# Optimization experiments

Measured on AMD Instinct MI355X. Metric: run time of the kernel, lower is better.

## Reference

```python
import jax, jax.numpy as jnp
import numpy as np

B, N, S, T, D, H, DH, FF = 16, 300, 300, 77, 512, 8, 64, 2048
L = T + S + N
XPOS_SCALE_BASE = 512.0


def _ln(v):
    m = v.mean(-1, keepdims=True)
    var = v.var(-1, keepdims=True)
    return (v - m) * jax.lax.rsqrt(var + 1e-6)


def _rms(v, g):
    return v * jax.lax.rsqrt(jnp.mean(v * v, axis=-1, keepdims=True) + 1e-6) * g


def _rotate_half(v):
    half = v.shape[-1] // 2
    v2 = v.reshape(v.shape[:-1] + (half, 2))
    return jnp.stack([-v2[..., 1], v2[..., 0]], axis=-1).reshape(v.shape)


def _rope_xpos(q, k):
    # lucidrains RotaryEmbedding(dim=64, use_xpos=True).rotate_queries_and_keys
    Dh = q.shape[-1]
    Lq = q.shape[-2]
    inv = 1.0 / (10000.0 ** (jnp.arange(0, Dh, 2, dtype=jnp.float32) / Dh))
    t = jnp.arange(Lq, dtype=jnp.float32)
    ang = jnp.repeat(t[:, None] * inv[None, :], 2, axis=-1)  # [L, Dh]
    base = (jnp.arange(0, Dh, 2, dtype=jnp.float32) + 0.4 * Dh) / (1.4 * Dh)
    power = (t - Lq // 2) / XPOS_SCALE_BASE
    scale = jnp.repeat(base[None, :] ** power[:, None], 2, axis=-1)  # [L, Dh]
    cos, sin = jnp.cos(ang), jnp.sin(ang)
    qo = q * (cos * scale) + _rotate_half(q) * (sin * scale)
    ko = k * (cos / scale) + _rotate_half(k) * (sin / scale)
    return qo, ko


def _fwd(x, src, txt, temb, Wqkv, bqkv, Wo, bo, gqk, Wada, bada, Wff1, bff1, Wff2, bff2, pos_q, pos_k, valid):
    Bb = x.shape[0]
    # AdaLayerNormZero modulation per stream (0=hidden, 1=source, 2=text)
    ada = jnp.einsum('bd,sde->sbe', jax.nn.silu(temb), Wada) + bada[:, None, :]  # [3,B,6D]
    sh_a, sc_a, g_a, sh_m, sc_m, g_m = jnp.split(ada, 6, axis=-1)  # each [3,B,D]

    streams = [x, src, txt]
    qs, ks_, vs = [], [], []
    for i, s_ in enumerate(streams):
        n = _ln(s_) * (1.0 + sc_a[i][:, None, :]) + sh_a[i][:, None, :]
        q = (n @ Wqkv[i, 0] + bqkv[i, 0]).reshape(Bb, -1, H, DH).transpose(0, 2, 1, 3)
        k = (n @ Wqkv[i, 1] + bqkv[i, 1]).reshape(Bb, -1, H, DH).transpose(0, 2, 1, 3)
        v = (n @ Wqkv[i, 2] + bqkv[i, 2]).reshape(Bb, -1, H, DH).transpose(0, 2, 1, 3)
        q = _rms(q, gqk[i, 0])
        k = _rms(k, gqk[i, 1])
        qs.append(q); ks_.append(k); vs.append(v)

    # rotary (xpos) on motion streams, learned pos-embed on text stream
    q0, k0 = _rope_xpos(qs[0], ks_[0])
    q1, k1 = _rope_xpos(qs[1], ks_[1])
    q2 = qs[2] + pos_q[None, None, :, :]
    k2 = ks_[2] + pos_k[None, None, :, :]

    # concat order: [text, source, hidden]
    q = jnp.concatenate([q2, q1, q0], axis=2)
    k = jnp.concatenate([k2, k1, k0], axis=2)
    v = jnp.concatenate([vs[2], vs[1], vs[0]], axis=2)

    Lt = q.shape[2]
    vm = valid.astype(jnp.float32)
    mask = (vm[:, :, None] * vm[:, None, :]) > 0
    mask = mask | jnp.eye(Lt, dtype=bool)[None]  # compute_boolean_matrix
    bias = jnp.where(mask, 0.0, -jnp.inf)[:, None, :, :]

    scores = jnp.einsum('bhld,bhmd->bhlm', q, k) / jnp.sqrt(jnp.float32(DH)) + bias
    att = jax.nn.softmax(scores, axis=-1)
    o = jnp.einsum('bhlm,bhmd->bhld', att, v).transpose(0, 2, 1, 3).reshape(Bb, Lt, H * DH)

    Tl, Sl = txt.shape[1], src.shape[1]
    attouts = [o[:, Tl + Sl:], o[:, Tl:Tl + Sl], o[:, :Tl]]  # hidden, source, text
    outs = []
    for i, (s_, ao) in enumerate(zip(streams, attouts)):
        a = ao @ Wo[i] + bo[i]
        h = s_ + g_a[i][:, None, :] * a
        n2 = _ln(h) * (1.0 + sc_m[i][:, None, :]) + sh_m[i][:, None, :]
        u = n2 @ Wff1[i] + bff1[i]
        lin, gate = jnp.split(u, 2, axis=-1)
        ff = (lin * jax.nn.gelu(gate, approximate=False)) @ Wff2[i] + bff2[i]
        outs.append(h + g_m[i][:, None, :] * ff)
    # return concat [text, source, hidden]
    return jnp.concatenate([outs[2], outs[1], outs[0]], axis=1)


def setup_inputs() -> dict:
    key = jax.random.key(0)
    ks = jax.random.split(key, 20)
    p = lambda k, shp: jax.random.normal(k, shp, jnp.float32) * 0.02
    return {
        'x': jax.random.normal(ks[0], (B, N, D), jnp.float32),
        'src': jax.random.normal(ks[1], (B, S, D), jnp.float32),
        'txt': jax.random.normal(ks[2], (B, T, D), jnp.float32),
        'temb': jax.random.normal(ks[3], (B, D), jnp.float32),
        'Wqkv': p(ks[4], (3, 3, D, D)),
        'bqkv': p(ks[5], (3, 3, D)),
        'Wo': p(ks[6], (3, D, D)),
        'bo': p(ks[7], (3, D)),
        'gqk': jnp.ones((3, 2, DH), jnp.float32),
        'Wada': p(ks[8], (3, D, 6 * D)),
        'bada': p(ks[9], (3, 6 * D)),
        'Wff1': p(ks[10], (3, D, 2 * FF)),
        'bff1': p(ks[11], (3, 2 * FF)),
        'Wff2': p(ks[12], (3, FF, D)),
        'bff2': p(ks[13], (3, D)),
        'pos_q': p(ks[14], (T, DH)),
        'pos_k': p(ks[15], (T, DH)),
        'valid': jax.random.randint(ks[16], (B, L), 0, 2, dtype=jnp.int32),
    }


def reference(x, src, txt, temb, Wqkv, bqkv, Wo, bo, gqk, Wada, bada, Wff1, bff1, Wff2, bff2, pos_q, pos_k, valid):
    return _fwd(x, src, txt, temb, Wqkv, bqkv, Wo, bo, gqk, Wada, bada, Wff1, bff1, Wff2, bff2, pos_q, pos_k, valid)
```

## Files before the change

### kernel.cpp

```cpp
#include <hip/hip_runtime.h>
#include <math.h>

#define DEV __device__ __forceinline__

typedef short bf8 __attribute__((ext_vector_type(8)));
typedef float f32x4 __attribute__((ext_vector_type(4)));

#define TOK 10832

DEV unsigned short f2bf(float f) {
  union { float f; unsigned u; } x; x.f = f;
  unsigned r = x.u + 0x7fffu + ((x.u >> 16) & 1u);
  return (unsigned short)(r >> 16);
}
DEV float bf2f(unsigned short h) {
  union { unsigned u; float f; } x; x.u = ((unsigned)h) << 16; return x.f;
}
DEV unsigned cvtpk(float lo, float hi) {
  unsigned r;
  asm("v_cvt_pk_bf16_f32 %0, %1, %2" : "=v"(r) : "v"(lo), "v"(hi));
  return r;
}
DEV void decode_row(int row, int& s, int& b, int& p) {
  if (row < 4800)      { s = 0; b = row / 300; p = row - b * 300; }
  else if (row < 9600) { s = 1; int r = row - 4800; b = r / 300; p = r - b * 300; }
  else                 { s = 2; int r = row - 9600; b = r / 77;  p = r - b * 77; }
}
DEV f32x4 MFMA(bf8 a, bf8 b, f32x4 c) {
  return __builtin_amdgcn_mfma_f32_16x16x32_bf16(a, b, c, 0, 0, 0);
}
DEV void gld16(const unsigned short* g, unsigned short* l) {
  __builtin_amdgcn_global_load_lds((const __attribute__((address_space(1))) unsigned int*)g,
                                   (__attribute__((address_space(3))) unsigned int*)l,
                                   16, 0, 0);
}
DEV void vmdrain() { asm volatile("s_waitcnt vmcnt(0)" ::: "memory"); }

__global__ __launch_bounds__(256) void k_transpose(const float* __restrict__ src,
                                                   unsigned short* __restrict__ dst,
                                                   int R, int C, long sstride, long dstride) {
  __shared__ float t[32][33];
  const float* s = src + (long)blockIdx.z * sstride;
  unsigned short* d = dst + (long)blockIdx.z * dstride;
  int c0 = blockIdx.x * 32, r0 = blockIdx.y * 32;
  int tx = threadIdx.x, ty = threadIdx.y;
  #pragma unroll
  for (int i = ty; i < 32; i += 8) t[i][tx] = s[(long)(r0 + i) * C + c0 + tx];
  __syncthreads();
  #pragma unroll
  for (int i = ty; i < 32; i += 8) d[(long)(c0 + i) * R + r0 + tx] = f2bf(t[tx][i]);
}

__global__ __launch_bounds__(256) void k_ada1(const float* __restrict__ temb,
    const float* __restrict__ Wada, float* __restrict__ part) {
  __shared__ float st[16][64];
  int s = blockIdx.y, kc = blockIdx.z;
  int e = blockIdx.x * 256 + threadIdx.x;
  int d0 = kc * 64;
  for (int i = threadIdx.x; i < 16 * 64; i += 256) {
    int b = i >> 6, d = i & 63;
    float v = temb[b * 512 + d0 + d];
    st[b][d] = v / (1.f + __expf(-v));
  }
  __syncthreads();
  float acc[16];
  #pragma unroll
  for (int b = 0; b < 16; b++) acc[b] = 0.f;
  const float* wp = Wada + (long)s * 512 * 3072 + (long)d0 * 3072 + e;
  for (int d = 0; d < 64; d++) {
    float wv = wp[(long)d * 3072];
    #pragma unroll
    for (int b = 0; b < 16; b++) acc[b] += st[b][d] * wv;
  }
  float* pp = part + (((long)kc * 3 + s) * 16) * 3072 + e;
  #pragma unroll
  for (int b = 0; b < 16; b++) pp[(long)b * 3072] = acc[b];
}

__global__ __launch_bounds__(256) void k_ada2(const float* __restrict__ part,
    const float* __restrict__ bada, float* __restrict__ ada) {
  int idx = blockIdx.x * 256 + threadIdx.x;
  int e = idx % 3072, sb = idx / 3072, s = sb >> 4;
  float a = bada[s * 3072 + e];
  #pragma unroll
  for (int kc = 0; kc < 8; kc++) a += part[((long)kc * 48 + sb) * 3072 + e];
  ada[idx] = a;
}

__global__ __launch_bounds__(256) void k_rope_tab(float* __restrict__ rc,
    float* __restrict__ rs, float* __restrict__ rsc) {
  int i = blockIdx.x * 256 + threadIdx.x;
  if (i >= 300 * 32) return;
  int p = i >> 5, f = i & 31;
  float inv = powf(10000.f, -(2.f * f) / 64.f);
  float ang = (float)p * inv;
  float base = (2.f * f + 25.6f) / 89.6f;
  float pw = (float)(p - 150) * (1.f / 512.f);
  rc[i] = cosf(ang);
  rs[i] = sinf(ang);
  rsc[i] = powf(base, pw);
}

__global__ __launch_bounds__(256) void k_padzero(unsigned short* __restrict__ qb,
    unsigned short* __restrict__ kb, unsigned short* __restrict__ vtb) {
  int bh = blockIdx.x, t = threadIdx.x;
  for (int i = t; i < 27 * 64; i += 256) {
    int r = 677 + (i >> 6), c = i & 63;
    long idx = ((long)bh * 704 + r) * 64 + c;
    qb[idx] = 0; kb[idx] = 0;
  }
  for (int i = t; i < 64 * 27; i += 256) {
    int r = i / 27, c = 677 + (i - r * 27);
    vtb[((long)bh * 64 + r) * 704 + c] = 0;
  }
}

__global__ __launch_bounds__(256) void k_lnmod(const float* __restrict__ xp,
    const float* __restrict__ sp, const float* __restrict__ tp,
    const float* __restrict__ hbuf, const float* __restrict__ ada,
    unsigned short* __restrict__ outp, int chunk) {
  int row = blockIdx.x;
  int s, b, p; decode_row(row, s, b, p);
  const float* in;
  if (hbuf) in = hbuf + (long)row * 512;
  else {
    const float* basep = (s == 0) ? xp : (s == 1) ? sp : tp;
    int len = (s == 2) ? 77 : 300;
    in = basep + ((long)b * len + p) * 512;
  }
  int t = threadIdx.x;
  float v0 = in[t], v1 = in[t + 256];
  float s1 = v0 + v1, s2 = v0 * v0 + v1 * v1;
  #pragma unroll
  for (int d = 32; d; d >>= 1) { s1 += __shfl_xor(s1, d); s2 += __shfl_xor(s2, d); }
  __shared__ float r1[4], r2[4];
  int wid = t >> 6, lane = t & 63;
  if (lane == 0) { r1[wid] = s1; r2[wid] = s2; }
  __syncthreads();
  float S = r1[0] + r1[1] + r1[2] + r1[3];
  float Q = r2[0] + r2[1] + r2[2] + r2[3];
  float mean = S * (1.f / 512.f);
  float var = Q * (1.f / 512.f) - mean * mean;
  float rstd = rsqrtf(var + 1e-6f);
  const float* ap = ada + ((long)s * 16 + b) * 3072 + chunk * 512;
  float sh0 = ap[t], sh1 = ap[t + 256];
  float sc0 = ap[512 + t], sc1 = ap[512 + t + 256];
  long ob = (long)row * 512;
  outp[ob + t]       = f2bf((v0 - mean) * rstd * (1.f + sc0) + sh0);
  outp[ob + t + 256] = f2bf((v1 - mean) * rstd * (1.f + sc1) + sh1);
}

template <int EPI>
__global__ __launch_bounds__(256) void k_gemm128(const unsigned short* __restrict__ A,
    const unsigned short* __restrict__ Wt, const float* __restrict__ bias,
    float* __restrict__ outF, unsigned short* __restrict__ outB,
    const float* __restrict__ hread, const float* __restrict__ ada,
    const float* __restrict__ xp, const float* __restrict__ sp, const float* __restrict__ tp,
    int K, int N) {
  int s = blockIdx.z;
  int mt = blockIdx.y;
  int Mtiles = (s == 2) ? 10 : 38;
  if (mt >= Mtiles) return;
  int Ms = (s == 2) ? 1232 : 4800;
  int rowbase = s * 4800;
  int m0 = mt * 128, n0 = blockIdx.x * 128;
  __shared__ unsigned short As[2][4096];
  __shared__ unsigned short Bs[2][4096];
  int tid = threadIdx.x;
  int w = tid >> 6, lane = tid & 63;
  int wr = w >> 1, wc = w & 1;
  int l16 = lane & 15, lg = lane >> 4;
  const unsigned short* Ag = A + (long)rowbase * K;
  const unsigned short* Bg = Wt + (long)s * N * K;
  int lrow = lane >> 2, lcol = (lane & 3) * 8;
  int ar[2], br[2];
  #pragma unroll
  for (int rnd = 0; rnd < 2; rnd++) {
    int rr = (w * 2 + rnd) * 16 + lrow;
    int a_ = m0 + rr; if (a_ >= Ms) a_ = Ms - 1;
    ar[rnd] = a_;
    br[rnd] = n0 + rr;
  }
  f32x4 acc[4][4];
  #pragma unroll
  for (int i = 0; i < 4; i++)
    #pragma unroll
    for (int j = 0; j < 4; j++) acc[i][j] = (f32x4){0.f, 0.f, 0.f, 0.f};
  #pragma unroll
  for (int rnd = 0; rnd < 2; rnd++) {
    gld16(Ag + (long)ar[rnd] * K + lcol, &As[0][(w * 2 + rnd) * 512]);
    gld16(Bg + (long)br[rnd] * K + lcol, &Bs[0][(w * 2 + rnd) * 512]);
  }
  vmdrain();
  __syncthreads();
  int buf = 0;
  for (int k0 = 0; k0 < K; k0 += 32) {
    int nx = k0 + 32;
    if (nx < K) {
      #pragma unroll
      for (int rnd = 0; rnd < 2; rnd++) {
        gld16(Ag + (long)ar[rnd] * K + nx + lcol, &As[buf ^ 1][(w * 2 + rnd) * 512]);
        gld16(Bg + (long)br[rnd] * K + nx + lcol, &Bs[buf ^ 1][(w * 2 + rnd) * 512]);
      }
    }
    bf8 af[4], bv[4];
    #pragma unroll
    for (int i = 0; i < 4; i++) {
      af[i] = *(const bf8*)&As[buf][(wr * 64 + i * 16 + l16) * 32 + lg * 8];
      bv[i] = *(const bf8*)&Bs[buf][(wc * 64 + i * 16 + l16) * 32 + lg * 8];
    }
    #pragma unroll
    for (int i = 0; i < 4; i++)
      #pragma unroll
      for (int j = 0; j < 4; j++)
        acc[i][j] = MFMA(af[i], bv[j], acc[i][j]);
    vmdrain();
    __syncthreads();
    buf ^= 1;
  }
  #pragma unroll
  for (int i = 0; i < 4; i++) {
    #pragma unroll
    for (int r = 0; r < 4; r++) {
      int rloc = m0 + wr * 64 + i * 16 + lg * 4 + r;
      if (rloc >= Ms) continue;
      int grow = rowbase + rloc;
      int b, p;
      if (s == 2) { b = rloc / 77;  p = rloc - b * 77; }
      else        { b = rloc / 300; p = rloc - b * 300; }
      #pragma unroll
      for (int j = 0; j < 4; j++) {
        int col = n0 + wc * 64 + j * 16 + l16;
        float v = acc[i][j][r] + bias[s * N + col];
        if constexpr (EPI == 0) {
          outB[(long)grow * 1536 + col] = f2bf(v);
        } else if constexpr (EPI == 1) {
          const float* basep = (s == 0) ? xp : (s == 1) ? sp : tp;
          int len = (s == 2) ? 77 : 300;
          float iv = basep[((long)b * len + p) * 512 + col];
          float ga = ada[((long)s * 16 + b) * 3072 + 1024 + col];
          outF[(long)grow * 512 + col] = iv + ga * v;
        } else {
          float hv = hread[(long)grow * 512 + col];
          float gm = ada[((long)s * 16 + b) * 3072 + 2560 + col];
          int l = ((s == 0) ? 377 : (s == 1) ? 77 : 0) + p;
          outF[((long)b * 677 + l) * 512 + col] = hv + gm * v;
        }
      }
    }
  }
}

__global__ __launch_bounds__(256) void k_geglu128(const unsigned short* __restrict__ A,
    const unsigned short* __restrict__ Wt, const float* __restrict__ bias,
    unsigned short* __restrict__ gout) {
  int s = blockIdx.z;
  int mt = blockIdx.y;
  int Mtiles = (s == 2) ? 10 : 38;
  if (mt >= Mtiles) return;
  int Ms = (s == 2) ? 1232 : 4800;
  int rowbase = s * 4800;
  int m0 = mt * 128, n0 = blockIdx.x * 64;
  __shared__ unsigned short As[2][4096];
  __shared__ unsigned short Bl[2][2048];
  __shared__ unsigned short Bg[2][2048];
  int tid = threadIdx.x;
  int w = tid >> 6, lane = tid & 63;
  int l16 = lane & 15, lg = lane >> 4;
  const unsigned short* Ag = A + (long)rowbase * 512;
  const unsigned short* Ws = Wt + (long)s * 4096 * 512;
  int lrow = lane >> 2, lcol = (lane & 3) * 8;
  int ar[2];
  #pragma unroll
  for (int rnd = 0; rnd < 2; rnd++) {
    int a_ = m0 + (w * 2 + rnd) * 16 + lrow; if (a_ >= Ms) a_ = Ms - 1;
    ar[rnd] = a_;
  }
  int blr = n0 + w * 16 + lrow;
  int bgr = 2048 + n0 + w * 16 + lrow;
  f32x4 accl[2][4], accg[2][4];
  #pragma unroll
  for (int i = 0; i < 2; i++)
    #pragma unroll
    for (int j = 0; j < 4; j++) {
      accl[i][j] = (f32x4){0.f, 0.f, 0.f, 0.f};
      accg[i][j] = (f32x4){0.f, 0.f, 0.f, 0.f};
    }
  #pragma unroll
  for (int rnd = 0; rnd < 2; rnd++)
    gld16(Ag + (long)ar[rnd] * 512 + lcol, &As[0][(w * 2 + rnd) * 512]);
  gld16(Ws + (long)blr * 512 + lcol, &Bl[0][w * 512]);
  gld16(Ws + (long)bgr * 512 + lcol, &Bg[0][w * 512]);
  vmdrain();
  __syncthreads();
  int buf = 0;
  for (int k0 = 0; k0 < 512; k0 += 32) {
    int nx = k0 + 32;
    if (nx < 512) {
      #pragma unroll
      for (int rnd = 0; rnd < 2; rnd++)
        gld16(Ag + (long)ar[rnd] * 512 + nx + lcol, &As[buf ^ 1][(w * 2 + rnd) * 512]);
      gld16(Ws + (long)blr * 512 + nx + lcol, &Bl[buf ^ 1][w * 512]);
      gld16(Ws + (long)bgr * 512 + nx + lcol, &Bg[buf ^ 1][w * 512]);
    }
    bf8 af[2], bl[4], bg[4];
    #pragma unroll
    for (int i = 0; i < 2; i++)
      af[i] = *(const bf8*)&As[buf][(w * 32 + i * 16 + l16) * 32 + lg * 8];
    #pragma unroll
    for (int j = 0; j < 4; j++) {
      bl[j] = *(const bf8*)&Bl[buf][(j * 16 + l16) * 32 + lg * 8];
      bg[j] = *(const bf8*)&Bg[buf][(j * 16 + l16) * 32 + lg * 8];
    }
    #pragma unroll
    for (int i = 0; i < 2; i++)
      #pragma unroll
      for (int j = 0; j < 4; j++) {
        accl[i][j] = MFMA(af[i], bl[j], accl[i][j]);
        accg[i][j] = MFMA(af[i], bg[j], accg[i][j]);
      }
    vmdrain();
    __syncthreads();
    buf ^= 1;
  }
  #pragma unroll
  for (int i = 0; i < 2; i++) {
    #pragma unroll
    for (int r = 0; r < 4; r++) {
      int rloc = m0 + w * 32 + i * 16 + lg * 4 + r;
      if (rloc >= Ms) continue;
      int grow = rowbase + rloc;
      #pragma unroll
      for (int j = 0; j < 4; j++) {
        int col = n0 + j * 16 + l16;
        float lv = accl[i][j][r] + bias[s * 4096 + col];
        float gv = accg[i][j][r] + bias[s * 4096 + 2048 + col];
        float g  = lv * 0.5f * gv * (1.f + erff(gv * 0.70710678118654752f));
        gout[(long)grow * 2048 + col] = f2bf(g);
      }
    }
  }
}

__global__ __launch_bounds__(256) void k_rmsrope(const unsigned short* __restrict__ qkv,
    const float* __restrict__ gqk, const float* __restrict__ posq, const float* __restrict__ posk,
    const float* __restrict__ rcos, const float* __restrict__ rsin, const float* __restrict__ rscl,
    unsigned short* __restrict__ qb, unsigned short* __restrict__ kb,
    unsigned short* __restrict__ vtb) {
  int gw = (blockIdx.x * 256 + threadIdx.x) >> 6;
  int lane = threadIdx.x & 63;
  int token = gw >> 3, h = gw & 7;
  if (token >= TOK) return;
  int s, b, p; decode_row(token, s, b, p);
  long base = (long)token * 1536 + h * 64 + lane;
  float q = bf2f(qkv[base]);
  float k = bf2f(qkv[base + 512]);
  float v = bf2f(qkv[base + 1024]);
  float sq = q * q, sk = k * k;
  #pragma unroll
  for (int d = 32; d; d >>= 1) { sq += __shfl_xor(sq, d); sk += __shfl_xor(sk, d); }
  q *= rsqrtf(sq * (1.f / 64.f) + 1e-6f) * gqk[s * 128 + lane];
  k *= rsqrtf(sk * (1.f / 64.f) + 1e-6f) * gqk[s * 128 + 64 + lane];
  int l;
  if (s == 2) {
    l = p;
    q += posq[p * 64 + lane];
    k += posk[p * 64 + lane];
  } else {
    l = (s == 1 ? 77 : 377) + p;
    int pr = lane >> 1;
    float c = rcos[p * 32 + pr], sn = rsin[p * 32 + pr], sc = rscl[p * 32 + pr];
    float qo = __shfl_xor(q, 1), ko = __shfl_xor(k, 1);
    float sgn = (lane & 1) ? 1.f : -1.f;
    q = (q * c + sgn * qo * sn) * sc;
    k = (k * c + sgn * ko * sn) / sc;
  }
  long bh = (long)(b * 8 + h);
  long qi = (bh * 704 + l) * 64 + lane;
  qb[qi] = f2bf(q);
  kb[qi] = f2bf(k);
  vtb[(bh * 64 + lane) * 704 + l] = f2bf(v);
}

__global__ __launch_bounds__(512, 8) void k_attn(const unsigned short* __restrict__ qb,
    const unsigned short* __restrict__ kb, const unsigned short* __restrict__ vtb,
    const int* __restrict__ valid, unsigned short* __restrict__ ob) {
  __shared__ unsigned short Kb[2][4096];
  __shared__ unsigned short Vb[2][4096];
  __shared__ unsigned char maskv[704];
  int f0 = blockIdx.x;
  int fp = (f0 & 7) * 96 + (f0 >> 3);
  int bh = fp / 6, qtile = fp - bh * 6;
  int b = bh >> 3, h = bh & 7;
  int tid = threadIdx.x;
  for (int i = tid; i < 704; i += 512)
    maskv[i] = (i < 677) ? (unsigned char)(valid[b * 677 + i] != 0) : (unsigned char)0;
  int w = tid >> 6, lane = tid & 63;
  int l16 = lane & 15, lg = lane >> 4;
  int qt = qtile * 128 + w * 16;
  int qrow = qt + l16;
  int qrc = qrow > 703 ? 703 : qrow;
  const unsigned short* qbase = qb + (long)bh * 704 * 64;
  const unsigned short* kbase = kb + (long)bh * 704 * 64;
  const unsigned short* vbase = vtb + (long)bh * 64 * 704;
  bf8 qf0 = *(const bf8*)(qbase + qrc * 64 + lg * 8);
  bf8 qf1 = *(const bf8*)(qbase + qrc * 64 + 32 + lg * 8);
  int scol = (((lane & 7) << 4) ^ ((lane >> 3) << 4)) >> 1;
  int srow = w * 8 + (lane >> 3);
  const unsigned short* ksrc = kbase + srow * 64 + scol;
  const unsigned short* vsrc = vbase + srow * 704 + scol;
  unsigned short* kd0 = &Kb[0][w * 512];
  unsigned short* kd1 = &Kb[1][w * 512];
  unsigned short* vd0 = &Vb[0][w * 512];
  unsigned short* vd1 = &Vb[1][w * 512];
  gld16(ksrc, kd0);
  gld16(vsrc, vd0);
  vmdrain();
  __syncthreads();
  int mq = maskv[qrc];
  int sw = (l16 & 7) << 4;
  float lsum = 0.f;
  f32x4 Oc[4];
  #pragma unroll
  for (int df = 0; df < 4; df++) Oc[df] = (f32x4){0.f, 0.f, 0.f, 0.f};
  union U { bf8 v; unsigned u[4]; uint2 d[2]; };
  int buf = 0;
  for (int t = 0; t < 11; t++) {
    if (t < 10) {
      int ktn = (t + 1) * 64;
      gld16(ksrc + ktn * 64, buf ? kd0 : kd1);
      gld16(vsrc + ktn, buf ? vd0 : vd1);
    }
    int kt = t * 64;
    const unsigned short* Kc = Kb[buf];
    const unsigned short* Vc = Vb[buf];
    float psum = 0.f;
    unsigned pk[4][2];
    #pragma unroll
    for (int f = 0; f < 4; f++) {
      int row = f * 16 + l16;
      f32x4 sa = (f32x4){0.f, 0.f, 0.f, 0.f};
      sa = MFMA(*(const bf8*)&Kc[(row * 128 + ((lg * 16) ^ sw)) >> 1], qf0, sa);
      sa = MFMA(*(const bf8*)&Kc[(row * 128 + ((lg * 16 + 64) ^ sw)) >> 1], qf1, sa);
      unsigned mw = *(const unsigned*)&maskv[kt + f * 16 + lg * 4];
      float pr[4];
      #pragma unroll
      for (int r = 0; r < 4; r++) {
        int key = kt + f * 16 + lg * 4 + r;
        bool ok = ((mq & (mw >> (8 * r))) & 1) || (key == qrow);
        float sv = ok ? fmaf(sa[r], 0.125f, -20.f) : -1e30f;
        float pv = __expf(sv);
        pr[r] = pv;
        psum += pv;
      }
      pk[f][0] = cvtpk(pr[0], pr[1]);
      pk[f][1] = cvtpk(pr[2], pr[3]);
    }
    psum += __shfl_xor(psum, 16);
    psum += __shfl_xor(psum, 32);
    lsum += psum;
    #pragma unroll
    for (int c = 0; c < 2; c++) {
      U pu;
      pu.u[0] = pk[2 * c][0]; pu.u[1] = pk[2 * c][1];
      pu.u[2] = pk[2 * c + 1][0]; pu.u[3] = pk[2 * c + 1][1];
      #pragma unroll
      for (int df = 0; df < 4; df++) {
        int row = df * 16 + l16;
        U vu;
        vu.d[0] = *(const uint2*)&Vc[(row * 128 + ((c * 64 + lg * 8) ^ sw)) >> 1];
        vu.d[1] = *(const uint2*)&Vc[(row * 128 + ((c * 64 + lg * 8 + 32) ^ sw)) >> 1];
        Oc[df] = MFMA(vu.v, pu.v, Oc[df]);
      }
    }
    vmdrain();
    __syncthreads();
    buf ^= 1;
  }
  if (qrow < 677) {
    float inv = 1.f / fmaxf(lsum, 1e-30f);
    int l = qrow;
    int orow = (l < 77) ? 9600 + b * 77 + l
             : (l < 377) ? 4800 + b * 300 + (l - 77)
                         : b * 300 + (l - 377);
    unsigned short* op = ob + (long)orow * 512 + h * 64;
    #pragma unroll
    for (int df = 0; df < 4; df++) {
      uint2 st;
      st.x = cvtpk(Oc[df][0] * inv, Oc[df][1] * inv);
      st.y = cvtpk(Oc[df][2] * inv, Oc[df][3] * inv);
      *(uint2*)(op + df * 16 + lg * 4) = st;
    }
  }
}

extern "C" void kernel_launch(void* const* d_in, const int* in_sizes, int n_in,
                              void* d_out, int out_size, void* d_ws, size_t ws_size,
                              hipStream_t stream) {
  const float* xp   = (const float*)d_in[0];
  const float* sp   = (const float*)d_in[1];
  const float* tp   = (const float*)d_in[2];
  const float* temb = (const float*)d_in[3];
  const float* Wqkv = (const float*)d_in[4];
  const float* bqkv = (const float*)d_in[5];
  const float* Wo   = (const float*)d_in[6];
  const float* bo   = (const float*)d_in[7];
  const float* gqk  = (const float*)d_in[8];
  const float* Wada = (const float*)d_in[9];
  const float* bada = (const float*)d_in[10];
  const float* Wff1 = (const float*)d_in[11];
  const float* bff1 = (const float*)d_in[12];
  const float* Wff2 = (const float*)d_in[13];
  const float* bff2 = (const float*)d_in[14];
  const float* posq = (const float*)d_in[15];
  const float* posk = (const float*)d_in[16];
  const int*   valid= (const int*)d_in[17];
  float* out = (float*)d_out;

  char* w = (char*)d_ws;
  size_t off = 0;
  auto take = [&](size_t bytes) -> char* {
    char* p = w + off;
    off = (off + bytes + 255) & ~(size_t)255;
    return p;
  };
  unsigned short* wqkvT = (unsigned short*)take(3UL * 1536 * 512 * 2);
  unsigned short* woT   = (unsigned short*)take(3UL * 512 * 512 * 2);
  unsigned short* wff1T = (unsigned short*)take(3UL * 4096 * 512 * 2);
  unsigned short* wff2T = (unsigned short*)take(3UL * 512 * 2048 * 2);
  float*          adab  = (float*)take(3UL * 16 * 3072 * 4);
  float*          adap  = (float*)take(8UL * 3 * 16 * 3072 * 4);
  float*          rcosb = (float*)take(300UL * 32 * 4);
  float*          rsinb = (float*)take(300UL * 32 * 4);
  float*          rsclb = (float*)take(300UL * 32 * 4);
  unsigned short* nbuf  = (unsigned short*)take((size_t)TOK * 512 * 2);
  unsigned short* qkvb  = (unsigned short*)take((size_t)TOK * 1536 * 2);
  unsigned short* qbf   = (unsigned short*)take(16UL * 8 * 704 * 64 * 2);
  unsigned short* kbf   = (unsigned short*)take(16UL * 8 * 704 * 64 * 2);
  unsigned short* vtb   = (unsigned short*)take(16UL * 8 * 64 * 704 * 2);
  unsigned short* obuf  = (unsigned short*)take((size_t)TOK * 512 * 2);
  float*          hb    = (float*)take((size_t)TOK * 512 * 4);
  unsigned short* n2b   = (unsigned short*)take((size_t)TOK * 512 * 2);
  unsigned short* gbuf  = (unsigned short*)take((size_t)TOK * 2048 * 2);
  (void)ws_size; (void)in_sizes; (void)n_in; (void)out_size;

  k_transpose<<<dim3(16, 16, 9), dim3(32, 8), 0, stream>>>(Wqkv, wqkvT, 512, 512, 262144L, 262144L);
  k_transpose<<<dim3(16, 16, 3), dim3(32, 8), 0, stream>>>(Wo, woT, 512, 512, 262144L, 262144L);
  k_transpose<<<dim3(128, 16, 3), dim3(32, 8), 0, stream>>>(Wff1, wff1T, 512, 4096, 2097152L, 2097152L);
  k_transpose<<<dim3(16, 64, 3), dim3(32, 8), 0, stream>>>(Wff2, wff2T, 2048, 512, 1048576L, 1048576L);
  k_ada1<<<dim3(12, 3, 8), 256, 0, stream>>>(temb, Wada, adap);
  k_ada2<<<576, 256, 0, stream>>>(adap, bada, adab);
  k_rope_tab<<<38, 256, 0, stream>>>(rcosb, rsinb, rsclb);
  k_padzero<<<128, 256, 0, stream>>>(qbf, kbf, vtb);
  k_lnmod<<<TOK, 256, 0, stream>>>(xp, sp, tp, nullptr, adab, nbuf, 0);
  k_gemm128<0><<<dim3(12, 38, 3), 256, 0, stream>>>(nbuf, wqkvT, bqkv, nullptr, qkvb, nullptr,
                                                    adab, xp, sp, tp, 512, 1536);
  k_rmsrope<<<21664, 256, 0, stream>>>(qkvb, gqk, posq, posk, rcosb, rsinb, rsclb, qbf, kbf, vtb);
  k_attn<<<768, 512, 0, stream>>>(qbf, kbf, vtb, valid, obuf);
  k_gemm128<1><<<dim3(4, 38, 3), 256, 0, stream>>>(obuf, woT, bo, hb, nullptr, nullptr,
                                                   adab, xp, sp, tp, 512, 512);
  k_lnmod<<<TOK, 256, 0, stream>>>(xp, sp, tp, hb, adab, n2b, 3);
  k_geglu128<<<dim3(32, 38, 3), 256, 0, stream>>>(n2b, wff1T, bff1, gbuf);
  k_gemm128<2><<<dim3(4, 38, 3), 256, 0, stream>>>(gbuf, wff2T, bff2, out, nullptr, hb,
                                                   adab, xp, sp, tp, 2048, 512);
}
```

Baseline: 470.8 us.

## Merge prep kernels into one launch and triple-buffer GEMM LDS pipelines

```diff
diff --git a/kernel.cpp b/kernel.cpp
--- a/kernel.cpp
+++ b/kernel.cpp
@@ -35,46 +35,99 @@
                                    16, 0, 0);
 }
 DEV void vmdrain() { asm volatile("s_waitcnt vmcnt(0)" ::: "memory"); }
-
-__global__ __launch_bounds__(256) void k_transpose(const float* __restrict__ src,
-                                                   unsigned short* __restrict__ dst,
-                                                   int R, int C, long sstride, long dstride) {
-  __shared__ float t[32][33];
-  const float* s = src + (long)blockIdx.z * sstride;
-  unsigned short* d = dst + (long)blockIdx.z * dstride;
-  int c0 = blockIdx.x * 32, r0 = blockIdx.y * 32;
-  int tx = threadIdx.x, ty = threadIdx.y;
-  #pragma unroll
-  for (int i = ty; i < 32; i += 8) t[i][tx] = s[(long)(r0 + i) * C + c0 + tx];
+DEV void pipe_bar4() {
+  asm volatile("s_waitcnt vmcnt(4) lgkmcnt(0)" ::: "memory");
+  __builtin_amdgcn_s_barrier();
+  __builtin_amdgcn_sched_barrier(0);
+}
+DEV void pipe_bar0() {
+  asm volatile("s_waitcnt vmcnt(0) lgkmcnt(0)" ::: "memory");
+  __builtin_amdgcn_s_barrier();
+  __builtin_amdgcn_sched_barrier(0);
+}
+
+DEV void tr32(const float* __restrict__ src, unsigned short* __restrict__ dst,
+              int R, int C, int cx, int cy, int tid, float* sh) {
+  int tx = tid & 31, ty = tid >> 5;
+  int c0 = cx * 32, r0 = cy * 32;
+  #pragma unroll
+  for (int i = ty; i < 32; i += 8) sh[i * 33 + tx] = src[(long)(r0 + i) * C + c0 + tx];
   __syncthreads();
   #pragma unroll
-  for (int i = ty; i < 32; i += 8) d[(long)(c0 + i) * R + r0 + tx] = f2bf(t[tx][i]);
-}
-
-__global__ __launch_bounds__(256) void k_ada1(const float* __restrict__ temb,
-    const float* __restrict__ Wada, float* __restrict__ part) {
-  __shared__ float st[16][64];
-  int s = blockIdx.y, kc = blockIdx.z;
-  int e = blockIdx.x * 256 + threadIdx.x;
-  int d0 = kc * 64;
-  for (int i = threadIdx.x; i < 16 * 64; i += 256) {
-    int b = i >> 6, d = i & 63;
-    float v = temb[b * 512 + d0 + d];
-    st[b][d] = v / (1.f + __expf(-v));
-  }
-  __syncthreads();
-  float acc[16];
-  #pragma unroll
-  for (int b = 0; b < 16; b++) acc[b] = 0.f;
-  const float* wp = Wada + (long)s * 512 * 3072 + (long)d0 * 3072 + e;
-  for (int d = 0; d < 64; d++) {
-    float wv = wp[(long)d * 3072];
-    #pragma unroll
-    for (int b = 0; b < 16; b++) acc[b] += st[b][d] * wv;
-  }
-  float* pp = part + (((long)kc * 3 + s) * 16) * 3072 + e;
-  #pragma unroll
-  for (int b = 0; b < 16; b++) pp[(long)b * 3072] = acc[b];
+  for (int i = ty; i < 32; i += 8) dst[(long)(c0 + i) * R + r0 + tx] = f2bf(sh[tx * 33 + i]);
+}
+
+__global__ __launch_bounds__(256) void k_prep(
+    const float* __restrict__ Wqkv, const float* __restrict__ Wo,
+    const float* __restrict__ Wff1, const float* __restrict__ Wff2,
+    unsigned short* __restrict__ wqkvT, unsigned short* __restrict__ woT,
+    unsigned short* __restrict__ wff1T, unsigned short* __restrict__ wff2T,
+    unsigned short* __restrict__ qb, unsigned short* __restrict__ kb,
+    unsigned short* __restrict__ vtb,
+    float* __restrict__ rc, float* __restrict__ rs, float* __restrict__ rsc,
+    const float* __restrict__ temb, const float* __restrict__ Wada,
+    float* __restrict__ part) {
+  __shared__ float sh[32 * 33];
+  int i = blockIdx.x, tid = threadIdx.x;
+  if (i < 2304) {
+    int z = i >> 8, r = i & 255;
+    tr32(Wqkv + (long)z * 262144, wqkvT + (long)z * 262144, 512, 512, r & 15, r >> 4, tid, sh);
+  } else if (i < 3072) {
+    int j = i - 2304; int z = j >> 8, r = j & 255;
+    tr32(Wo + (long)z * 262144, woT + (long)z * 262144, 512, 512, r & 15, r >> 4, tid, sh);
+  } else if (i < 9216) {
+    int j = i - 3072; int z = j >> 11, r = j & 2047;
+    tr32(Wff1 + (long)z * 2097152, wff1T + (long)z * 2097152, 512, 4096, r & 127, r >> 7, tid, sh);
+  } else if (i < 12288) {
+    int j = i - 9216; int z = j >> 10, r = j & 1023;
+    tr32(Wff2 + (long)z * 1048576, wff2T + (long)z * 1048576, 2048, 512, r & 15, r >> 4, tid, sh);
+  } else if (i < 12416) {
+    int bh = i - 12288;
+    for (int q = tid; q < 27 * 64; q += 256) {
+      int r = 677 + (q >> 6), c = q & 63;
+      long idx = ((long)bh * 704 + r) * 64 + c;
+      qb[idx] = 0; kb[idx] = 0;
+    }
+    for (int q = tid; q < 64 * 27; q += 256) {
+      int r = q / 27, c = 677 + (q - r * 27);
+      vtb[((long)bh * 64 + r) * 704 + c] = 0;
+    }
+  } else if (i < 12454) {
+    int q = (i - 12416) * 256 + tid;
+    if (q < 300 * 32) {
+      int p = q >> 5, f = q & 31;
+      float inv = powf(10000.f, -(2.f * f) / 64.f);
+      float ang = (float)p * inv;
+      float base = (2.f * f + 25.6f) / 89.6f;
+      float pw = (float)(p - 150) * (1.f / 512.f);
+      rc[q] = cosf(ang);
+      rs[q] = sinf(ang);
+      rsc[q] = powf(base, pw);
+    }
+  } else {
+    int j = i - 12454;
+    int ex = j % 12, rest = j / 12, s = rest % 3, kc = rest / 3;
+    int d0 = kc * 64;
+    for (int q = tid; q < 16 * 64; q += 256) {
+      int b = q >> 6, d = q & 63;
+      float v = temb[b * 512 + d0 + d];
+      sh[(b << 6) + d] = v / (1.f + __expf(-v));
+    }
+    __syncthreads();
+    int e = ex * 256 + tid;
+    float acc[16];
+    #pragma unroll
+    for (int b = 0; b < 16; b++) acc[b] = 0.f;
+    const float* wp = Wada + (long)s * 512 * 3072 + (long)d0 * 3072 + e;
+    for (int d = 0; d < 64; d++) {
+      float wv = wp[(long)d * 3072];
+      #pragma unroll
+      for (int b = 0; b < 16; b++) acc[b] += sh[(b << 6) + d] * wv;
+    }
+    float* pp = part + (((long)kc * 3 + s) * 16) * 3072 + e;
+    #pragma unroll
+    for (int b = 0; b < 16; b++) pp[(long)b * 3072] = acc[b];
+  }
 }
 
 __global__ __launch_bounds__(256) void k_ada2(const float* __restrict__ part,
@@ -85,34 +138,6 @@
   #pragma unroll
   for (int kc = 0; kc < 8; kc++) a += part[((long)kc * 48 + sb) * 3072 + e];
   ada[idx] = a;
-}
-
-__global__ __launch_bounds__(256) void k_rope_tab(float* __restrict__ rc,
-    float* __restrict__ rs, float* __restrict__ rsc) {
-  int i = blockIdx.x * 256 + threadIdx.x;
-  if (i >= 300 * 32) return;
-  int p = i >> 5, f = i & 31;
-  float inv = powf(10000.f, -(2.f * f) / 64.f);
-  float ang = (float)p * inv;
-  float base = (2.f * f + 25.6f) / 89.6f;
-  float pw = (float)(p - 150) * (1.f / 512.f);
-  rc[i] = cosf(ang);
-  rs[i] = sinf(ang);
-  rsc[i] = powf(base, pw);
-}
-
-__global__ __launch_bounds__(256) void k_padzero(unsigned short* __restrict__ qb,
-    unsigned short* __restrict__ kb, unsigned short* __restrict__ vtb) {
-  int bh = blockIdx.x, t = threadIdx.x;
-  for (int i = t; i < 27 * 64; i += 256) {
-    int r = 677 + (i >> 6), c = i & 63;
-    long idx = ((long)bh * 704 + r) * 64 + c;
-    qb[idx] = 0; kb[idx] = 0;
-  }
-  for (int i = t; i < 64 * 27; i += 256) {
-    int r = i / 27, c = 677 + (i - r * 27);
-    vtb[((long)bh * 64 + r) * 704 + c] = 0;
-  }
 }
 
 __global__ __launch_bounds__(256) void k_lnmod(const float* __restrict__ xp,
@@ -164,8 +189,8 @@
   int Ms = (s == 2) ? 1232 : 4800;
   int rowbase = s * 4800;
   int m0 = mt * 128, n0 = blockIdx.x * 128;
-  __shared__ unsigned short As[2][4096];
-  __shared__ unsigned short Bs[2][4096];
+  __shared__ unsigned short As[3][4096];
+  __shared__ unsigned short Bs[3][4096];
   int tid = threadIdx.x;
   int w = tid >> 6, lane = tid & 63;
   int wr = w >> 1, wc = w & 1;
@@ -181,42 +206,40 @@
     ar[rnd] = a_;
     br[rnd] = n0 + rr;
   }
+  auto stage = [&](int kt, int bufi) {
+    #pragma unroll
+    for (int rnd = 0; rnd < 2; rnd++) {
+      gld16(Ag + (long)ar[rnd] * K + kt + lcol, &As[bufi][(w * 2 + rnd) * 512]);
+      gld16(Bg + (long)br[rnd] * K + kt + lcol, &Bs[bufi][(w * 2 + rnd) * 512]);
+    }
+  };
   f32x4 acc[4][4];
   #pragma unroll
   for (int i = 0; i < 4; i++)
     #pragma unroll
     for (int j = 0; j < 4; j++) acc[i][j] = (f32x4){0.f, 0.f, 0.f, 0.f};
-  #pragma unroll
-  for (int rnd = 0; rnd < 2; rnd++) {
-    gld16(Ag + (long)ar[rnd] * K + lcol, &As[0][(w * 2 + rnd) * 512]);
-    gld16(Bg + (long)br[rnd] * K + lcol, &Bs[0][(w * 2 + rnd) * 512]);
-  }
-  vmdrain();
-  __syncthreads();
-  int buf = 0;
-  for (int k0 = 0; k0 < K; k0 += 32) {
-    int nx = k0 + 32;
-    if (nx < K) {
-      #pragma unroll
-      for (int rnd = 0; rnd < 2; rnd++) {
-        gld16(Ag + (long)ar[rnd] * K + nx + lcol, &As[buf ^ 1][(w * 2 + rnd) * 512]);
-        gld16(Bg + (long)br[rnd] * K + nx + lcol, &Bs[buf ^ 1][(w * 2 + rnd) * 512]);
-      }
+  int nt = K >> 5;
+  stage(0, 0);
+  stage(32, 1);
+  int bi = 0;
+  for (int t = 0; t < nt; ++t) {
+    if (t == nt - 1) pipe_bar0(); else pipe_bar4();
+    if (t + 2 < nt) {
+      int b2 = bi + 2; if (b2 >= 3) b2 -= 3;
+      stage((t + 2) << 5, b2);
     }
     bf8 af[4], bv[4];
     #pragma unroll
     for (int i = 0; i < 4; i++) {
-      af[i] = *(const bf8*)&As[buf][(wr * 64 + i * 16 + l16) * 32 + lg * 8];
-      bv[i] = *(const bf8*)&Bs[buf][(wc * 64 + i * 16 + l16) * 32 + lg * 8];
+      af[i] = *(const bf8*)&As[bi][(wr * 64 + i * 16 + l16) * 32 + lg * 8];
+      bv[i] = *(const bf8*)&Bs[bi][(wc * 64 + i * 16 + l16) * 32 + lg * 8];
     }
     #pragma unroll
     for (int i = 0; i < 4; i++)
       #pragma unroll
       for (int j = 0; j < 4; j++)
         acc[i][j] = MFMA(af[i], bv[j], acc[i][j]);
-    vmdrain();
-    __syncthreads();
-    buf ^= 1;
+    bi = (bi + 1 == 3) ? 0 : bi + 1;
   }
   #pragma unroll
   for (int i = 0; i < 4; i++) {
@@ -261,9 +284,9 @@
   int Ms = (s == 2) ? 1232 : 4800;
   int rowbase = s * 4800;
   int m0 = mt * 128, n0 = blockIdx.x * 64;
-  __shared__ unsigned short As[2][4096];
-  __shared__ unsigned short Bl[2][2048];
-  __shared__ unsigned short Bg[2][2048];
+  __shared__ unsigned short As[3][4096];
+  __shared__ unsigned short Bl[3][2048];
+  __shared__ unsigned short Bg[3][2048];
   int tid = threadIdx.x;
   int w = tid >> 6, lane = tid & 63;
   int l16 = lane & 15, lg = lane >> 4;
@@ -278,6 +301,13 @@
   }
   int blr = n0 + w * 16 + lrow;
   int bgr = 2048 + n0 + w * 16 + lrow;
+  auto stage = [&](int kt, int bufi) {
+    #pragma unroll
+    for (int rnd = 0; rnd < 2; rnd++)
+      gld16(Ag + (long)ar[rnd] * 512 + kt + lcol, &As[bufi][(w * 2 + rnd) * 512]);
+    gld16(Ws + (long)blr * 512 + kt + lcol, &Bl[bufi][w * 512]);
+    gld16(Ws + (long)bgr * 512 + kt + lcol, &Bg[bufi][w * 512]);
+  };
   f32x4 accl[2][4], accg[2][4];
   #pragma unroll
   for (int i = 0; i < 2; i++)
@@ -286,31 +316,23 @@
       accl[i][j] = (f32x4){0.f, 0.f, 0.f, 0.f};
       accg[i][j] = (f32x4){0.f, 0.f, 0.f, 0.f};
     }
-  #pragma unroll
-  for (int rnd = 0; rnd < 2; rnd++)
-    gld16(Ag + (long)ar[rnd] * 512 + lcol, &As[0][(w * 2 + rnd) * 512]);
-  gld16(Ws + (long)blr * 512 + lcol, &Bl[0][w * 512]);
-  gld16(Ws + (long)bgr * 512 + lcol, &Bg[0][w * 512]);
-  vmdrain();
-  __syncthreads();
-  int buf = 0;
-  for (int k0 = 0; k0 < 512; k0 += 32) {
-    int nx = k0 + 32;
-    if (nx < 512) {
-      #pragma unroll
-      for (int rnd = 0; rnd < 2; rnd++)
-        gld16(Ag + (long)ar[rnd] * 512 + nx + lcol, &As[buf ^ 1][(w * 2 + rnd) * 512]);
-      gld16(Ws + (long)blr * 512 + nx + lcol, &Bl[buf ^ 1][w * 512]);
-      gld16(Ws + (long)bgr * 512 + nx + lcol, &Bg[buf ^ 1][w * 512]);
+  stage(0, 0);
+  stage(32, 1);
+  int bi = 0;
+  for (int t = 0; t < 16; ++t) {
+    if (t == 15) pipe_bar0(); else pipe_bar4();
+    if (t + 2 < 16) {
+      int b2 = bi + 2; if (b2 >= 3) b2 -= 3;
+      stage((t + 2) << 5, b2);
     }
     bf8 af[2], bl[4], bg[4];
     #pragma unroll
     for (int i = 0; i < 2; i++)
-      af[i] = *(const bf8*)&As[buf][(w * 32 + i * 16 + l16) * 32 + lg * 8];
+      af[i] = *(const bf8*)&As[bi][(w * 32 + i * 16 + l16) * 32 + lg * 8];
     #pragma unroll
     for (int j = 0; j < 4; j++) {
-      bl[j] = *(const bf8*)&Bl[buf][(j * 16 + l16) * 32 + lg * 8];
-      bg[j] = *(const bf8*)&Bg[buf][(j * 16 + l16) * 32 + lg * 8];
+      bl[j] = *(const bf8*)&Bl[bi][(j * 16 + l16) * 32 + lg * 8];
+      bg[j] = *(const bf8*)&Bg[bi][(j * 16 + l16) * 32 + lg * 8];
     }
     #pragma unroll
     for (int i = 0; i < 2; i++)
@@ -319,9 +341,7 @@
         accl[i][j] = MFMA(af[i], bl[j], accl[i][j]);
         accg[i][j] = MFMA(af[i], bg[j], accg[i][j]);
       }
-    vmdrain();
-    __syncthreads();
-    buf ^= 1;
+    bi = (bi + 1 == 3) ? 0 : bi + 1;
   }
   #pragma unroll
   for (int i = 0; i < 2; i++) {
@@ -544,14 +564,9 @@
   unsigned short* gbuf  = (unsigned short*)take((size_t)TOK * 2048 * 2);
   (void)ws_size; (void)in_sizes; (void)n_in; (void)out_size;
 
-  k_transpose<<<dim3(16, 16, 9), dim3(32, 8), 0, stream>>>(Wqkv, wqkvT, 512, 512, 262144L, 262144L);
-  k_transpose<<<dim3(16, 16, 3), dim3(32, 8), 0, stream>>>(Wo, woT, 512, 512, 262144L, 262144L);
-  k_transpose<<<dim3(128, 16, 3), dim3(32, 8), 0, stream>>>(Wff1, wff1T, 512, 4096, 2097152L, 2097152L);
-  k_transpose<<<dim3(16, 64, 3), dim3(32, 8), 0, stream>>>(Wff2, wff2T, 2048, 512, 1048576L, 1048576L);
-  k_ada1<<<dim3(12, 3, 8), 256, 0, stream>>>(temb, Wada, adap);
+  k_prep<<<12742, 256, 0, stream>>>(Wqkv, Wo, Wff1, Wff2, wqkvT, woT, wff1T, wff2T,
+                                    qbf, kbf, vtb, rcosb, rsinb, rsclb, temb, Wada, adap);
   k_ada2<<<576, 256, 0, stream>>>(adap, bada, adab);
-  k_rope_tab<<<38, 256, 0, stream>>>(rcosb, rsinb, rsclb);
-  k_padzero<<<128, 256, 0, stream>>>(qbf, kbf, vtb);
   k_lnmod<<<TOK, 256, 0, stream>>>(xp, sp, tp, nullptr, adab, nbuf, 0);
   k_gemm128<0><<<dim3(12, 38, 3), 256, 0, stream>>>(nbuf, wqkvT, bqkv, nullptr, qkvb, nullptr,
                                                     adab, xp, sp, tp, 512, 1536);
```

Result: no change. 476.7 us (+1.3%).
